# Kernel optimization log

Measured on AMD Instinct MI355X. Metric: run time of the kernel, lower is better.

## Reference

```python
import jax, jax.numpy as jnp
import numpy as np

B, S, E, H = 2, 2048, 1024, 16
Dh = E // H  # 64
KEEP = 0.9   # 1 - dropout_p
INV_SCALE = 1.0  # forward() default; call site does not pass inv_scale


def setup_inputs() -> dict:
    key = jax.random.key(0)
    ks = jax.random.split(key, 12)
    query = jax.random.normal(ks[0], (B, S, E), dtype=jnp.float32)
    key_t = jax.random.normal(ks[1], (B, S, E), dtype=jnp.float32)
    value = jax.random.normal(ks[2], (B, S, E), dtype=jnp.float32)
    attn_mask = jax.random.randint(ks[3], (B, S), 0, 2, dtype=jnp.int32)
    # pre-scaled inverted dropout keep-mask (deterministic stand-in for F.dropout)
    dropout_mask = (jax.random.uniform(ks[4], (B, H, S, S)) < KEEP).astype(jnp.float32) / KEEP
    Wq = jax.random.normal(ks[5], (E, E), dtype=jnp.float32) * 0.02
    bq = jnp.zeros((E,), dtype=jnp.float32)
    Wk = jax.random.normal(ks[6], (E, E), dtype=jnp.float32) * 0.02
    bk = jnp.zeros((E,), dtype=jnp.float32)
    Wv = jax.random.normal(ks[7], (E, E), dtype=jnp.float32) * 0.02
    bv = jnp.zeros((E,), dtype=jnp.float32)
    return {"query": query, "key": key_t, "value": value, "attn_mask": attn_mask,
            "dropout_mask": dropout_mask, "Wq": Wq, "bq": bq, "Wk": Wk, "bk": bk,
            "Wv": Wv, "bv": bv}


def _heads(x, W, b):
    # Linear then split heads: (B,S,E) -> (B,H,S,Dh)
    y = x @ W.T + b
    return y.reshape(B, S, H, Dh).transpose(0, 2, 1, 3)


def reference(query, key, value, attn_mask, dropout_mask, Wq, bq, Wk, bk, Wv, bv):
    q = _heads(query, Wq, bq)
    k = _heads(key, Wk, bk)
    v = _heads(value, Wv, bv)
    scores = jnp.einsum("bhqd,bhkd->bhqk", q, k) / INV_SCALE
    pad = (attn_mask == 0)[:, None, None, :]  # (B,1,1,S) True = masked
    scores = jnp.where(pad, -jnp.inf, scores)
    attn = jax.nn.softmax(scores, axis=-1) * dropout_mask
    out = jnp.einsum("bhqk,bhkd->bhqd", attn, v)  # (B,H,S,Dh)
    return out
```

## Files before the change

kernel.cpp:

```cpp
#include <hip/hip_runtime.h>

#define B_ 2
#define S_ 2048
#define E_ 1024
#define H_ 16
#define DH 64
#define MM (B_*S_)
#define BHN (B_*H_)

typedef unsigned short u16;
typedef unsigned int u32;
typedef __attribute__((ext_vector_type(8))) __bf16 bf16x8;
typedef __attribute__((ext_vector_type(4))) float f32x4;
typedef __attribute__((ext_vector_type(8))) u16 u16x8;
typedef __attribute__((ext_vector_type(4))) u16 u16x4;

static __device__ __forceinline__ u16 f2bf(float f) {
  u32 u = __builtin_bit_cast(u32, f);
  u += 0x7fffu + ((u >> 16) & 1u);
  return (u16)(u >> 16);
}
static __device__ __forceinline__ float bf2f(u16 h) {
  return __builtin_bit_cast(float, (u32)h << 16);
}
static __device__ __forceinline__ u32 sw(u32 byte) {
  return byte ^ (((byte >> 7) & 7u) << 4);
}
static __device__ __forceinline__ bf16x8 frag(const u16* lds, u32 byte) {
  return *(const bf16x8*)((const char*)lds + byte);
}
static __device__ __forceinline__ f32x4 mfma16(bf16x8 a, bf16x8 b, f32x4 c) {
  return __builtin_amdgcn_mfma_f32_16x16x32_bf16(a, b, c, 0, 0, 0);
}
static __device__ __forceinline__ void gload_lds16(const u16* g, u16* lds_base) {
  __builtin_amdgcn_global_load_lds(
      (const __attribute__((address_space(1))) u32*)g,
      (__attribute__((address_space(3))) u32*)lds_base, 16, 0, 0);
}

struct SplitArg { const float* s; u16* h; u16* l; int n4; };

__global__ void split6_kernel(SplitArg a0, SplitArg a1, SplitArg a2,
                              SplitArg a3, SplitArg a4, SplitArg a5) {
  SplitArg A = (blockIdx.z == 0) ? a0 : (blockIdx.z == 1) ? a1 : (blockIdx.z == 2) ? a2
             : (blockIdx.z == 3) ? a3 : (blockIdx.z == 4) ? a4 : a5;
  int i = blockIdx.x * blockDim.x + threadIdx.x;
  int stride = gridDim.x * blockDim.x;
  for (; i < A.n4; i += stride) {
    float4 v = ((const float4*)A.s)[i];
    u16x4 h, l;
    h.x = f2bf(v.x); l.x = f2bf(v.x - bf2f(h.x));
    h.y = f2bf(v.y); l.y = f2bf(v.y - bf2f(h.y));
    h.z = f2bf(v.z); l.z = f2bf(v.z - bf2f(h.z));
    h.w = f2bf(v.w); l.w = f2bf(v.w - bf2f(h.w));
    ((u16x4*)A.h)[i] = h;
    ((u16x4*)A.l)[i] = l;
  }
}

struct ProjArgs {
  const u16* xhi; const u16* xlo; const u16* whi; const u16* wlo;
  const float* bias; u16* ohi; u16* olo; int mode;
};

__global__ __launch_bounds__(256, 2) void proj_gemm(ProjArgs a0, ProjArgs a1, ProjArgs a2) {
  ProjArgs A = (blockIdx.z == 0) ? a0 : (blockIdx.z == 1) ? a1 : a2;
  __shared__ u16 As[128 * 64];
  __shared__ u16 Bs[128 * 64];
  const int t = threadIdx.x;
  const int l = t & 63, wid = t >> 6;
  const int g = l >> 4, ln = l & 15;
  const int wm = wid >> 1, wn = wid & 1;
  int bid = blockIdx.y * 8 + blockIdx.x;
  int sid = (bid & 7) * 32 + (bid >> 3);
  const int m0 = (sid >> 3) * 128, e0 = (sid & 7) * 128;

  f32x4 acc[4][4] = {};
  const int nkt = (A.mode == 2) ? 32 : 48;

  for (int kt = 0; kt < nkt; ++kt) {
    int kp = kt * 64;
    const u16* asrc = (kp < 2048) ? A.xhi : A.xlo;
    const u16* bsrc = (kp < 1024 || kp >= 2048) ? A.whi : A.wlo;
    int kc = kp & 1023;
#pragma unroll
    for (int r = 0; r < 4; ++r) {
      int cr = wid * 4 + r;
      int row = cr * 8 + (l >> 3);
      int col = (l & 7) * 8;
      gload_lds16(asrc + (size_t)(m0 + row) * 1024 + kc + col, As + cr * 512);
      gload_lds16(bsrc + (size_t)(e0 + row) * 1024 + kc + col, Bs + cr * 512);
    }
    __syncthreads();
#pragma unroll
    for (int ks = 0; ks < 2; ++ks) {
      bf16x8 af[4], bfv[4];
#pragma unroll
      for (int i = 0; i < 4; ++i) {
        af[i] = frag(As, (u32)(wm * 64 + i * 16 + ln) * 128 + ks * 64 + g * 16);
        bfv[i] = frag(Bs, (u32)(wn * 64 + i * 16 + ln) * 128 + ks * 64 + g * 16);
      }
#pragma unroll
      for (int i = 0; i < 4; ++i)
#pragma unroll
        for (int j = 0; j < 4; ++j)
          acc[i][j] = mfma16(af[i], bfv[j], acc[i][j]);
    }
    __syncthreads();
  }

#pragma unroll
  for (int i = 0; i < 4; ++i) {
#pragma unroll
    for (int j = 0; j < 4; ++j) {
      int e = e0 + wn * 64 + j * 16 + ln;
      int h = e >> 6, d = e & 63;
      float bias = A.bias[e];
      if (A.mode < 2) {
#pragma unroll
        for (int r = 0; r < 4; ++r) {
          int m = m0 + wm * 64 + i * 16 + g * 4 + r;
          float v = acc[i][j][r] + bias;
          int b = m >> 11, s = m & 2047;
          size_t idx = ((size_t)((b * 16 + h) * 2048 + s)) * 64 + d;
          u16 hv = f2bf(v);
          A.ohi[idx] = hv;
          A.olo[idx] = f2bf(v - bf2f(hv));
        }
      } else {
        int m = m0 + wm * 64 + i * 16 + g * 4;
        int b = m >> 11, s = m & 2047;
        u16x4 pv;
#pragma unroll
        for (int r = 0; r < 4; ++r) pv[r] = f2bf(acc[i][j][r] + bias);
        size_t idx = ((size_t)((b * 16 + h) * 64 + d)) * 2048 + s;
        *(u16x4*)(A.ohi + idx) = pv;
      }
    }
  }
}

__global__ __launch_bounds__(256, 3) void attn_kernel(
    const u16* __restrict__ qhi, const u16* __restrict__ qlo,
    const u16* __restrict__ khi, const u16* __restrict__ klo,
    const u16* __restrict__ vt, const int* __restrict__ amask,
    const float* __restrict__ dmask, float* __restrict__ out) {
  __shared__ u16 Ksh[64 * 64];
  __shared__ u16 Ksl[64 * 64];
  __shared__ u16 Vs[64 * 64];
  __shared__ u16 Ps[4 * 16 * 64];

  const int t = threadIdx.x, l = t & 63, wid = t >> 6;
  const int g = l >> 4, ln = l & 15;

  int bid = blockIdx.y * 32 + blockIdx.x;
  int sid = (bid & 7) * 128 + (bid >> 3);
  const int qt = sid & 31, bh = sid >> 5, b = bh >> 4;
  const int q0 = qt * 64;
  const int qrow = q0 + wid * 16 + ln;
  const size_t qg = ((size_t)bh * 2048 + qrow) * 64;

  bf16x8 qh[2], ql[2];
#pragma unroll
  for (int ks = 0; ks < 2; ++ks) {
    qh[ks] = *(const bf16x8*)(qhi + qg + ks * 32 + g * 8);
    ql[ks] = *(const bf16x8*)(qlo + qg + ks * 32 + g * 8);
  }

  u16x8 rkh[2], rkl[2], rv[2];
  auto load_tile = [&](int kt) {
    const int k0 = kt * 64;
    const size_t kbase = ((size_t)bh * 2048 + k0) * 64;
#pragma unroll
    for (int i = 0; i < 2; ++i) {
      int c = t + 256 * i;
      rkh[i] = *(const u16x8*)(khi + kbase + c * 8);
      rkl[i] = *(const u16x8*)(klo + kbase + c * 8);
      int row = c >> 3;
      rv[i] = *(const u16x8*)(vt + ((size_t)bh * 64 + row) * 2048 + k0 + (c & 7) * 8);
    }
  };
  auto write_tile = [&]() {
#pragma unroll
    for (int i = 0; i < 2; ++i) {
      int c = t + 256 * i;
      u32 lb = sw((u32)c * 16);
      *(u16x8*)((char*)Ksh + lb) = rkh[i];
      *(u16x8*)((char*)Ksl + lb) = rkl[i];
      *(u16x8*)((char*)Vs + lb) = rv[i];
    }
  };

  load_tile(0);
  write_tile();
  __syncthreads();

  f32x4 O[4] = {};
  float Zacc = 0.f;
  const size_t dmrow = ((size_t)bh * 2048 + qrow) * 2048;
  const u32 psbase = (u32)(wid * 2048 + ln * 128);

  for (int kt = 0; kt < 32; ++kt) {
    const int k0 = kt * 64;
    load_tile(kt < 31 ? kt + 1 : 31);
    float4 dm[4]; int4 ok[4];
#pragma unroll
    for (int i = 0; i < 4; ++i) {
      dm[i] = *(const float4*)(dmask + dmrow + k0 + i * 16 + 4 * g);
      ok[i] = *(const int4*)(amask + b * 2048 + k0 + i * 16 + 4 * g);
    }

    f32x4 sc[4] = {};
#pragma unroll
    for (int ks = 0; ks < 2; ++ks) {
#pragma unroll
      for (int i = 0; i < 4; ++i) {
        u32 byt = sw((u32)((i * 16 + ln) * 128 + ks * 64 + g * 16));
        bf16x8 akh = frag(Ksh, byt);
        bf16x8 akl = frag(Ksl, byt);
        sc[i] = mfma16(akh, qh[ks], sc[i]);
        sc[i] = mfma16(akh, ql[ks], sc[i]);
        sc[i] = mfma16(akl, qh[ks], sc[i]);
      }
    }

#pragma unroll
    for (int i = 0; i < 4; ++i) {
      float e0 = ok[i].x ? __expf(sc[i][0]) : 0.f;
      float e1 = ok[i].y ? __expf(sc[i][1]) : 0.f;
      float e2 = ok[i].z ? __expf(sc[i][2]) : 0.f;
      float e3 = ok[i].w ? __expf(sc[i][3]) : 0.f;
      Zacc += (e0 + e1) + (e2 + e3);
      u16x4 p;
      p.x = f2bf(e0 * dm[i].x);
      p.y = f2bf(e1 * dm[i].y);
      p.z = f2bf(e2 * dm[i].z);
      p.w = f2bf(e3 * dm[i].w);
      *(u16x4*)((char*)Ps + sw(psbase + i * 32 + g * 8)) = p;
    }

#pragma unroll
    for (int ks = 0; ks < 2; ++ks) {
      bf16x8 bP = frag(Ps, sw(psbase + ks * 64 + g * 16));
#pragma unroll
      for (int id = 0; id < 4; ++id) {
        bf16x8 aV = frag(Vs, sw((u32)((id * 16 + ln) * 128 + ks * 64 + g * 16)));
        O[id] = mfma16(aV, bP, O[id]);
      }
    }

    __syncthreads();
    if (kt < 31) {
      write_tile();
      __syncthreads();
    }
  }

  float z = Zacc;
  z += __shfl_xor(z, 16, 64);
  z += __shfl_xor(z, 32, 64);
  float rz = 1.f / z;

#pragma unroll
  for (int id = 0; id < 4; ++id) {
    float4 o;
    o.x = O[id][0] * rz; o.y = O[id][1] * rz;
    o.z = O[id][2] * rz; o.w = O[id][3] * rz;
    *(float4*)(out + qg + id * 16 + 4 * g) = o;
  }
}

extern "C" void kernel_launch(void* const* d_in, const int* in_sizes, int n_in,
                              void* d_out, int out_size, void* d_ws, size_t ws_size,
                              hipStream_t stream) {
  const float* query = (const float*)d_in[0];
  const float* keyt  = (const float*)d_in[1];
  const float* value = (const float*)d_in[2];
  const int*   amask = (const int*)d_in[3];
  const float* dmask = (const float*)d_in[4];
  const float* Wq = (const float*)d_in[5];
  const float* bq = (const float*)d_in[6];
  const float* Wk = (const float*)d_in[7];
  const float* bk = (const float*)d_in[8];
  const float* Wv = (const float*)d_in[9];
  const float* bv = (const float*)d_in[10];

  char* ws = (char*)d_ws;
  size_t off = 0;
  auto alloc = [&](size_t bytes) {
    char* p = ws + off;
    off += (bytes + 255) & ~(size_t)255;
    return p;
  };
  const size_t XB = (size_t)MM * E_ * sizeof(u16);
  const size_t WB = (size_t)E_ * E_ * sizeof(u16);

  u16 *xh[3], *xl[3], *wh[3], *wl[3];
  for (int i = 0; i < 3; ++i) { xh[i] = (u16*)alloc(XB); xl[i] = (u16*)alloc(XB); }
  for (int i = 0; i < 3; ++i) { wh[i] = (u16*)alloc(WB); wl[i] = (u16*)alloc(WB); }
  u16* q_hi = (u16*)alloc(XB);
  u16* q_lo = (u16*)alloc(XB);
  u16* k_hi = (u16*)alloc(XB);
  u16* k_lo = (u16*)alloc(XB);
  u16* v_t  = (u16*)alloc(XB);
  if (off > ws_size) return;

  SplitArg sa[6] = {
      {query, xh[0], xl[0], MM * E_ / 4}, {keyt, xh[1], xl[1], MM * E_ / 4},
      {value, xh[2], xl[2], MM * E_ / 4}, {Wq, wh[0], wl[0], E_ * E_ / 4},
      {Wk, wh[1], wl[1], E_ * E_ / 4},    {Wv, wh[2], wl[2], E_ * E_ / 4},
  };
  split6_kernel<<<dim3(512, 1, 6), 256, 0, stream>>>(sa[0], sa[1], sa[2], sa[3], sa[4], sa[5]);

  ProjArgs pa[3] = {
      {xh[0], xl[0], wh[0], wl[0], bq, q_hi, q_lo, 0},
      {xh[1], xl[1], wh[1], wl[1], bk, k_hi, k_lo, 1},
      {xh[2], xl[2], wh[2], wl[2], bv, v_t, nullptr, 2},
  };
  proj_gemm<<<dim3(8, 32, 3), 256, 0, stream>>>(pa[0], pa[1], pa[2]);

  attn_kernel<<<dim3(32, 32), 256, 0, stream>>>(
      q_hi, q_lo, k_hi, k_lo, v_t, amask, dmask, (float*)d_out);
}
```

Before: 306.4 us.

## Prefetch dropout mask, bit-pack padding mask, fold log2e into Q, skip V low split

The change bit-packs the int padding mask in a tiny new kernel, so the attention loop reads two words per tile instead of int4 vectors. It prefetches the next tile's dropout-mask values one iteration ahead to hide their global-load latency. It also scales Q by log2(e) in the projection epilogue so exp2f can replace __expf, skips producing the unused low half of the value input, and raises proj_gemm launch bounds to 3 blocks. In exchange it adds register pressure from double-buffered dropout values and one extra kernel launch.

```diff
diff --git a/kernel.cpp b/kernel.cpp
--- a/kernel.cpp
+++ b/kernel.cpp
@@ -38,6 +38,8 @@
       (__attribute__((address_space(3))) u32*)lds_base, 16, 0, 0);
 }
 
+#define L2E 1.44269504088896340736f
+
 struct SplitArg { const float* s; u16* h; u16* l; int n4; };
 
 __global__ void split6_kernel(SplitArg a0, SplitArg a1, SplitArg a2,
@@ -46,15 +48,39 @@
              : (blockIdx.z == 3) ? a3 : (blockIdx.z == 4) ? a4 : a5;
   int i = blockIdx.x * blockDim.x + threadIdx.x;
   int stride = gridDim.x * blockDim.x;
-  for (; i < A.n4; i += stride) {
-    float4 v = ((const float4*)A.s)[i];
-    u16x4 h, l;
-    h.x = f2bf(v.x); l.x = f2bf(v.x - bf2f(h.x));
-    h.y = f2bf(v.y); l.y = f2bf(v.y - bf2f(h.y));
-    h.z = f2bf(v.z); l.z = f2bf(v.z - bf2f(h.z));
-    h.w = f2bf(v.w); l.w = f2bf(v.w - bf2f(h.w));
-    ((u16x4*)A.h)[i] = h;
-    ((u16x4*)A.l)[i] = l;
+  if (A.l) {
+    for (; i < A.n4; i += stride) {
+      float4 v = ((const float4*)A.s)[i];
+      u16x4 h, l;
+      h.x = f2bf(v.x); l.x = f2bf(v.x - bf2f(h.x));
+      h.y = f2bf(v.y); l.y = f2bf(v.y - bf2f(h.y));
+      h.z = f2bf(v.z); l.z = f2bf(v.z - bf2f(h.z));
+      h.w = f2bf(v.w); l.w = f2bf(v.w - bf2f(h.w));
+      ((u16x4*)A.h)[i] = h;
+      ((u16x4*)A.l)[i] = l;
+    }
+  } else {
+    for (; i < A.n4; i += stride) {
+      float4 v = ((const float4*)A.s)[i];
+      u16x4 h;
+      h.x = f2bf(v.x); h.y = f2bf(v.y); h.z = f2bf(v.z); h.w = f2bf(v.w);
+      ((u16x4*)A.h)[i] = h;
+    }
+  }
+}
+
+__global__ void pack_mask(const int* __restrict__ am, u32* __restrict__ pm) {
+  int w = threadIdx.x;
+  if (w < 128) {
+    int base = (w >> 6) * 2048 + (w & 63) * 32;
+    u32 bits = 0;
+#pragma unroll
+    for (int j = 0; j < 8; ++j) {
+      int4 v = *(const int4*)(am + base + j * 4);
+      bits |= (v.x ? 1u : 0u) << (4 * j) | (v.y ? 1u : 0u) << (4 * j + 1) |
+              (v.z ? 1u : 0u) << (4 * j + 2) | (v.w ? 1u : 0u) << (4 * j + 3);
+    }
+    pm[w] = bits;
   }
 }
 
@@ -63,7 +89,7 @@
   const float* bias; u16* ohi; u16* olo; int mode;
 };
 
-__global__ __launch_bounds__(256, 2) void proj_gemm(ProjArgs a0, ProjArgs a1, ProjArgs a2) {
+__global__ __launch_bounds__(256, 3) void proj_gemm(ProjArgs a0, ProjArgs a1, ProjArgs a2) {
   ProjArgs A = (blockIdx.z == 0) ? a0 : (blockIdx.z == 1) ? a1 : a2;
   __shared__ u16 As[128 * 64];
   __shared__ u16 Bs[128 * 64];
@@ -121,6 +147,7 @@
         for (int r = 0; r < 4; ++r) {
           int m = m0 + wm * 64 + i * 16 + g * 4 + r;
           float v = acc[i][j][r] + bias;
+          if (A.mode == 0) v *= L2E;
           int b = m >> 11, s = m & 2047;
           size_t idx = ((size_t)((b * 16 + h) * 2048 + s)) * 64 + d;
           u16 hv = f2bf(v);
@@ -143,7 +170,7 @@
 __global__ __launch_bounds__(256, 3) void attn_kernel(
     const u16* __restrict__ qhi, const u16* __restrict__ qlo,
     const u16* __restrict__ khi, const u16* __restrict__ klo,
-    const u16* __restrict__ vt, const int* __restrict__ amask,
+    const u16* __restrict__ vt, const u32* __restrict__ pm,
     const float* __restrict__ dmask, float* __restrict__ out) {
   __shared__ u16 Ksh[64 * 64];
   __shared__ u16 Ksl[64 * 64];
@@ -159,6 +186,7 @@
   const int q0 = qt * 64;
   const int qrow = q0 + wid * 16 + ln;
   const size_t qg = ((size_t)bh * 2048 + qrow) * 64;
+  const u32* pmb = pm + b * 64;
 
   bf16x8 qh[2], ql[2];
 #pragma unroll
@@ -166,6 +194,15 @@
     qh[ks] = *(const bf16x8*)(qhi + qg + ks * 32 + g * 8);
     ql[ks] = *(const bf16x8*)(qlo + qg + ks * 32 + g * 8);
   }
+
+  const size_t dmrow = ((size_t)bh * 2048 + qrow) * 2048;
+  float4 dmc[4], dmn[4];
+  auto load_dm = [&](int kt, float4* d) {
+    const int k0 = kt * 64;
+#pragma unroll
+    for (int i = 0; i < 4; ++i)
+      d[i] = *(const float4*)(dmask + dmrow + k0 + i * 16 + 4 * g);
+  };
 
   u16x8 rkh[2], rkl[2], rv[2];
   auto load_tile = [&](int kt) {
@@ -191,24 +228,21 @@
     }
   };
 
+  load_dm(0, dmc);
   load_tile(0);
   write_tile();
   __syncthreads();
 
   f32x4 O[4] = {};
   float Zacc = 0.f;
-  const size_t dmrow = ((size_t)bh * 2048 + qrow) * 2048;
   const u32 psbase = (u32)(wid * 2048 + ln * 128);
 
   for (int kt = 0; kt < 32; ++kt) {
-    const int k0 = kt * 64;
-    load_tile(kt < 31 ? kt + 1 : 31);
-    float4 dm[4]; int4 ok[4];
-#pragma unroll
-    for (int i = 0; i < 4; ++i) {
-      dm[i] = *(const float4*)(dmask + dmrow + k0 + i * 16 + 4 * g);
-      ok[i] = *(const int4*)(amask + b * 2048 + k0 + i * 16 + 4 * g);
-    }
+    if (kt < 31) {
+      load_dm(kt + 1, dmn);
+      load_tile(kt + 1);
+    }
+    u32 m0 = pmb[2 * kt], m1 = pmb[2 * kt + 1];
 
     f32x4 sc[4] = {};
 #pragma unroll
@@ -226,16 +260,17 @@
 
 #pragma unroll
     for (int i = 0; i < 4; ++i) {
-      float e0 = ok[i].x ? __expf(sc[i][0]) : 0.f;
-      float e1 = ok[i].y ? __expf(sc[i][1]) : 0.f;
-      float e2 = ok[i].z ? __expf(sc[i][2]) : 0.f;
-      float e3 = ok[i].w ? __expf(sc[i][3]) : 0.f;
+      u32 mm = (i < 2 ? m0 : m1) >> (((i & 1) << 4) + 4 * g);
+      float e0 = (mm & 1u) ? exp2f(sc[i][0]) : 0.f;
+      float e1 = (mm & 2u) ? exp2f(sc[i][1]) : 0.f;
+      float e2 = (mm & 4u) ? exp2f(sc[i][2]) : 0.f;
+      float e3 = (mm & 8u) ? exp2f(sc[i][3]) : 0.f;
       Zacc += (e0 + e1) + (e2 + e3);
       u16x4 p;
-      p.x = f2bf(e0 * dm[i].x);
-      p.y = f2bf(e1 * dm[i].y);
-      p.z = f2bf(e2 * dm[i].z);
-      p.w = f2bf(e3 * dm[i].w);
+      p.x = f2bf(e0 * dmc[i].x);
+      p.y = f2bf(e1 * dmc[i].y);
+      p.z = f2bf(e2 * dmc[i].z);
+      p.w = f2bf(e3 * dmc[i].w);
       *(u16x4*)((char*)Ps + sw(psbase + i * 32 + g * 8)) = p;
     }
 
@@ -253,6 +288,8 @@
     if (kt < 31) {
       write_tile();
       __syncthreads();
+#pragma unroll
+      for (int i = 0; i < 4; ++i) dmc[i] = dmn[i];
     }
   }
 
@@ -303,22 +340,24 @@
   u16* k_hi = (u16*)alloc(XB);
   u16* k_lo = (u16*)alloc(XB);
   u16* v_t  = (u16*)alloc(XB);
+  u32* pmask = (u32*)alloc(512);
   if (off > ws_size) return;
 
   SplitArg sa[6] = {
       {query, xh[0], xl[0], MM * E_ / 4}, {keyt, xh[1], xl[1], MM * E_ / 4},
-      {value, xh[2], xl[2], MM * E_ / 4}, {Wq, wh[0], wl[0], E_ * E_ / 4},
+      {value, xh[2], nullptr, MM * E_ / 4}, {Wq, wh[0], wl[0], E_ * E_ / 4},
       {Wk, wh[1], wl[1], E_ * E_ / 4},    {Wv, wh[2], wl[2], E_ * E_ / 4},
   };
   split6_kernel<<<dim3(512, 1, 6), 256, 0, stream>>>(sa[0], sa[1], sa[2], sa[3], sa[4], sa[5]);
+  pack_mask<<<1, 128, 0, stream>>>(amask, pmask);
 
   ProjArgs pa[3] = {
       {xh[0], xl[0], wh[0], wl[0], bq, q_hi, q_lo, 0},
       {xh[1], xl[1], wh[1], wl[1], bk, k_hi, k_lo, 1},
-      {xh[2], xl[2], wh[2], wl[2], bv, v_t, nullptr, 2},
+      {xh[2], nullptr, wh[2], wl[2], bv, v_t, nullptr, 2},
   };
   proj_gemm<<<dim3(8, 32, 3), 256, 0, stream>>>(pa[0], pa[1], pa[2]);
 
   attn_kernel<<<dim3(32, 32), 256, 0, stream>>>(
-      q_hi, q_lo, k_hi, k_lo, v_t, amask, dmask, (float*)d_out);
-}
+      q_hi, q_lo, k_hi, k_lo, v_t, pmask, dmask, (float*)d_out);
+}
```

New measurement: 294.7 us. 1.04x faster.
